# Kernel optimization log

Hardware: AMD Instinct MI355X
Metric: run time of the kernel (lower is better)

Reference implementation:

```python
import jax, jax.numpy as jnp
import numpy as np

HIDDEN = 1024
HEADS = 16
HEAD_DIM = HIDDEN // HEADS
B, S = 4, 2048


def setup_inputs() -> dict:
    key = jax.random.key(0)
    ks = jax.random.split(key, 12)
    d = {
        "query": jax.random.normal(ks[0], (B, S, HIDDEN), jnp.float32),
        "key": jax.random.normal(ks[1], (B, S, HIDDEN), jnp.float32),
        "value": jax.random.normal(ks[2], (B, S, HIDDEN), jnp.float32),
        "relative_time": jax.random.normal(ks[3], (B, 1, S, S), jnp.float32),
        # causal boolean mask (True = attend), matches masked_fill_(~mask)
        "attn_mask": jnp.broadcast_to(jnp.tril(jnp.ones((S, S), bool)), (B, S, S)),
    }
    scale = 1.0 / np.sqrt(HIDDEN)
    for i, name in enumerate(["q", "k", "v", "out"]):
        d[f"W{name}"] = jax.random.normal(ks[4 + 2 * i], (HIDDEN, HIDDEN), jnp.float32) * scale
        d[f"b{name}"] = jax.random.normal(ks[5 + 2 * i], (HIDDEN,), jnp.float32) * 0.01
    return d


def reference(query, key, value, relative_time, attn_mask,
              Wq, bq, Wk, bk, Wv, bv, Wout, bout):
    Bsz, Slen, _ = query.shape
    # linear projections (torch Linear: x @ W^T + b)
    Q = query @ Wq.T + bq
    K = key @ Wk.T + bk
    V = value @ Wv.T + bv
    # [B, H, S, Dh]
    Q = Q.reshape(Bsz, Slen, HEADS, HEAD_DIM).transpose(0, 2, 1, 3)
    K = K.reshape(Bsz, Slen, HEADS, HEAD_DIM).transpose(0, 2, 1, 3)
    V = V.reshape(Bsz, Slen, HEADS, HEAD_DIM).transpose(0, 2, 1, 3)

    scale = HEAD_DIM ** (-0.5)
    # scores: [B, H, S, S]; bias added BEFORE scaling, as in the original
    scores = jnp.einsum("bhqd,bhkd->bhqk", Q, K)
    scores = (scores + relative_time) * scale
    scores = jnp.where(attn_mask[:, None, :, :], scores, -jnp.inf)
    attn = jax.nn.softmax(scores, axis=-1)
    attn = jnp.nan_to_num(attn, nan=0.0)  # fully-masked rows -> 0
    # dropout: inference mode (training=False) -> identity
    out = jnp.einsum("bhqk,bhkd->bhqd", attn, V)
    out = out.transpose(0, 2, 1, 3).reshape(Bsz, Slen, HIDDEN)
    return out @ Wout.T + bout
```

## Files before the change

kernel.cpp:

```cpp
#include <hip/hip_runtime.h>


#define SEQ 2048
#define NH 16
#define DH 64
#define HID 1024
#define QSCALE 0.18033688011112f

typedef short bf16x8 __attribute__((ext_vector_type(8)));
typedef float f32x4  __attribute__((ext_vector_type(4)));
typedef unsigned short u16;
typedef unsigned short u16x4 __attribute__((ext_vector_type(4)));
typedef unsigned short u16x8 __attribute__((ext_vector_type(8)));

__device__ __forceinline__ float b2f(u16 u) {
    union { unsigned i; float f; } x; x.i = ((unsigned)u) << 16; return x.f;
}
__device__ __forceinline__ u16 f2b(float f) {
    union { float f; unsigned i; } x; x.f = f;
    unsigned r = x.i + 0x7fffu + ((x.i >> 16) & 1u);
    return (u16)(r >> 16);
}

typedef const __attribute__((address_space(1))) unsigned int guint;
typedef __attribute__((address_space(3))) unsigned int luint;
__device__ __forceinline__ void gload_lds16(const u16* g, u16* l) {
    __builtin_amdgcn_global_load_lds((guint*)g, (luint*)l, 16, 0, 0);
}

__global__ __launch_bounds__(256) void cvt_bf16_kernel(
    const float* __restrict__ in, u16* __restrict__ out, int n8)
{
    int i = blockIdx.x * 256 + threadIdx.x;
    const int stride = gridDim.x * 256;
    for (; i < n8; i += stride) {
        f32x4 a = *(const f32x4*)(in + (size_t)i * 8);
        f32x4 b = *(const f32x4*)(in + (size_t)i * 8 + 4);
        u16x8 o;
#pragma unroll
        for (int j = 0; j < 4; ++j) { o[j] = f2b(a[j]); o[j + 4] = f2b(b[j]); }
        *(u16x8*)(out + (size_t)i * 8) = o;
    }
}

__global__ __launch_bounds__(256) void rel_perm_kernel(
    const float* __restrict__ rel, u16* __restrict__ out)
{
    __shared__ u16 pl[4096];
    const int t   = threadIdx.x;
    const int blk = blockIdx.x;
    const int b   = blk >> 10;
    const int qc  = (blk >> 5) & 31;
    const int kc  = blk & 31;
    const int qloc  = t >> 2;
    const int kloc0 = (t & 3) << 4;

    const float* src = rel + ((size_t)b * SEQ + qc * 64 + qloc) * SEQ + kc * 64 + kloc0;
    const int qt   = qloc >> 4;
    const int quad = (qloc >> 2) & 3;
    const int g    = qloc & 3;
    const int nt   = t & 3;
    u16* dst = pl + qt * 1024 + quad * 256 + nt * 4 + g;
#pragma unroll
    for (int c = 0; c < 4; ++c) {
        f32x4 x = *(const f32x4*)(src + c * 4);
#pragma unroll
        for (int j = 0; j < 4; ++j)
            dst[(c * 4 + j) * 16] = f2b(x[j] * QSCALE);
    }
    __syncthreads();
    const size_t obase = (((size_t)b * 128 + qc * 4) * 32 + kc) * 1024;
#pragma unroll
    for (int q2 = 0; q2 < 4; ++q2)
        *(u16x4*)(out + obase + (size_t)q2 * 32768 + t * 4) =
            *(const u16x4*)(pl + q2 * 1024 + t * 4);
}

__global__ __launch_bounds__(256) void qkv_proj_kernel(
    const u16* __restrict__ xq, const u16* __restrict__ xk, const u16* __restrict__ xv,
    const u16* __restrict__ wq, const u16* __restrict__ wk, const u16* __restrict__ wv,
    const float* __restrict__ bq, const float* __restrict__ bk, const float* __restrict__ bv,
    u16* __restrict__ Qw, u16* __restrict__ Kw, u16* __restrict__ Vw)
{
    __shared__ __align__(16) u16 As[128 * 32];
    __shared__ __align__(16) u16 Bs[128 * 32];

    const int tid  = threadIdx.x;
    const int w    = tid >> 6;
    const int lane = tid & 63;
    const int l16  = lane & 15;
    const int quad = lane >> 4;

    const int bid = blockIdx.x;
    const int sel = bid >> 9;
    const int rem = bid & 511;
    const int tm = rem >> 3, tn = rem & 7;
    const int m0 = tm << 7, n0 = tn << 7;

    const u16* X    = sel == 0 ? xq : (sel == 1 ? xk : xv);
    const u16* W    = sel == 0 ? wq : (sel == 1 ? wk : wv);
    const float* bias = sel == 0 ? bq : (sel == 1 ? bk : bv);

    const int crow = lane >> 2;
    const int cofs = (lane & 3) << 3;

    f32x4 acc[4][4];
    const f32x4 zero = {0.f, 0.f, 0.f, 0.f};
#pragma unroll
    for (int r = 0; r < 4; ++r)
#pragma unroll
        for (int c = 0; c < 4; ++c) acc[r][c] = zero;

    const int wr = (w >> 1) << 6;
    const int wc = (w & 1) << 6;

    for (int k0 = 0; k0 < 1024; k0 += 32) {
#pragma unroll
        for (int c = 0; c < 2; ++c) {
            const int ch  = w + c * 4;
            const int row = ch * 16 + crow;
            gload_lds16(X + (size_t)(m0 + row) * 1024 + k0 + cofs, As + ch * 512 + lane * 8);
            gload_lds16(W + (size_t)(n0 + row) * 1024 + k0 + cofs, Bs + ch * 512 + lane * 8);
        }
        __syncthreads();
        bf16x8 a[4], b[4];
#pragma unroll
        for (int r = 0; r < 4; ++r) a[r] = *(const bf16x8*)(As + (wr + r * 16 + l16) * 32 + quad * 8);
#pragma unroll
        for (int c = 0; c < 4; ++c) b[c] = *(const bf16x8*)(Bs + (wc + c * 16 + l16) * 32 + quad * 8);
#pragma unroll
        for (int r = 0; r < 4; ++r)
#pragma unroll
            for (int c = 0; c < 4; ++c)
                acc[r][c] = __builtin_amdgcn_mfma_f32_16x16x32_bf16(a[r], b[c], acc[r][c], 0, 0, 0);
        __syncthreads();
    }

#pragma unroll
    for (int c = 0; c < 4; ++c) {
        const int n = n0 + wc + c * 16 + l16;
        const float bn = bias[n];
        const int h = n >> 6, d = n & 63;
#pragma unroll
        for (int r = 0; r < 4; ++r) {
#pragma unroll
            for (int g = 0; g < 4; ++g) {
                const int m  = m0 + wr + r * 16 + quad * 4 + g;
                const int b_ = m >> 11, s_ = m & 2047;
                const float val = acc[r][c][g] + bn;
                if (sel == 0)
                    Qw[(((size_t)(b_ * 16 + h)) * 2048 + s_) * 64 + d] = f2b(val * QSCALE);
                else if (sel == 1)
                    Kw[(((size_t)(b_ * 16 + h)) * 2048 + s_) * 64 + d] = f2b(val);
                else
                    Vw[(((size_t)(b_ * 16 + h)) * 64 + d) * 2048 + s_] = f2b(val);
            }
        }
    }
}

__global__ __launch_bounds__(512, 4) void attn_kernel(
    const u16* __restrict__ Qb, const u16* __restrict__ Kb,
    const u16* __restrict__ Vb, const u16* __restrict__ relb,
    u16* __restrict__ Ob)
{
    __shared__ __align__(16) u16 lds[18432];
    u16* Ks = lds;
    u16* Vt = lds + 4608;

    const int tid  = threadIdx.x;
    const int w    = tid >> 6;
    const int lane = tid & 63;
    const int l16  = lane & 15;
    const int quad = lane >> 4;
    u16* Pl = lds + 9216 + w * 1152;

    const int bh = blockIdx.x & 63;
    const int p  = blockIdx.x >> 6;
    const int b  = bh >> 4, h = bh & 15;

    const u16* Qp = Qb + (size_t)bh * SEQ * DH;
    const u16* Kg = Kb + (size_t)bh * SEQ * DH;
    const u16* Vg = Vb + (size_t)bh * DH * SEQ;

    const int r0 = tid >> 3, o0 = (tid & 7) << 3;

    for (int sidx = 0; sidx < 2; ++sidx) {
        const int qb  = sidx ? (15 - p) : p;
        const int q0w = qb * 128 + w * 16;

        bf16x8 qa[2];
#pragma unroll
        for (int ks = 0; ks < 2; ++ks)
            qa[ks] = *(const bf16x8*)(Qp + (size_t)(q0w + l16) * 64 + ks * 32 + quad * 8);

        f32x4 o[4], mrow, lrow;
        const f32x4 zero = {0.f, 0.f, 0.f, 0.f};
        const f32x4 ninf = {-1e30f, -1e30f, -1e30f, -1e30f};
        mrow = ninf; lrow = zero;
#pragma unroll
        for (int dt = 0; dt < 4; ++dt) o[dt] = zero;

        const int ntiles  = qb * 2 + 2;
        const int mytiles = qb * 2 + (w >> 2) + 1;

        const u16* relW = relb + ((size_t)(b * 128 + (q0w >> 4))) * 32768 + (size_t)lane * 16;

        bf16x8 kreg = *(const bf16x8*)(Kg + (size_t)r0 * 64 + o0);
        bf16x8 vreg = *(const bf16x8*)(Vg + (size_t)r0 * 2048 + o0);
        bf16x8 rr0 = *(const bf16x8*)(relW);
        bf16x8 rr1 = *(const bf16x8*)(relW + 8);

        for (int kt = 0; kt < ntiles; ++kt) {
            const int k0 = kt << 6;
            *(bf16x8*)(Ks + r0 * 72 + o0) = kreg;
            *(bf16x8*)(Vt + r0 * 72 + o0) = vreg;

            f32x4 s[4];
            if (kt < mytiles) {
#pragma unroll
                for (int nt = 0; nt < 4; ++nt)
#pragma unroll
                    for (int g = 0; g < 4; ++g)
                        s[nt][g] = b2f((u16)((nt < 2 ? rr0 : rr1)[(nt & 1) * 4 + g]));
            }

            const int ktn = (kt + 1 < ntiles) ? kt + 1 : kt;
            const int kn  = ktn << 6;
            kreg = *(const bf16x8*)(Kg + (size_t)(kn + r0) * 64 + o0);
            vreg = *(const bf16x8*)(Vg + (size_t)r0 * 2048 + kn + o0);
            rr0  = *(const bf16x8*)(relW + (size_t)ktn * 1024);
            rr1  = *(const bf16x8*)(relW + (size_t)ktn * 1024 + 8);
            __syncthreads();

            if (kt < mytiles) {
#pragma unroll
                for (int nt = 0; nt < 4; ++nt) {
                    bf16x8 kb0 = *(const bf16x8*)(Ks + (nt * 16 + l16) * 72 + quad * 8);
                    bf16x8 kb1 = *(const bf16x8*)(Ks + (nt * 16 + l16) * 72 + 32 + quad * 8);
                    s[nt] = __builtin_amdgcn_mfma_f32_16x16x32_bf16(qa[0], kb0, s[nt], 0, 0, 0);
                    s[nt] = __builtin_amdgcn_mfma_f32_16x16x32_bf16(qa[1], kb1, s[nt], 0, 0, 0);
                }
                if (kt == mytiles - 1) {
#pragma unroll
                    for (int nt = 0; nt < 4; ++nt)
#pragma unroll
                        for (int g = 0; g < 4; ++g) {
                            const int q = q0w + quad * 4 + g;
                            const int k = k0 + nt * 16 + l16;
                            if (k > q) s[nt][g] = -1e30f;
                        }
                }
                {
                    f32x4 t;
#pragma unroll
                    for (int g = 0; g < 4; ++g)
                        t[g] = fmaxf(fmaxf(s[0][g], s[1][g]), fmaxf(s[2][g], s[3][g]));
#pragma unroll
                    for (int off = 1; off < 16; off <<= 1)
#pragma unroll
                        for (int g = 0; g < 4; ++g)
                            t[g] = fmaxf(t[g], __shfl_xor(t[g], off, 64));
                    f32x4 mn, alpha;
#pragma unroll
                    for (int g = 0; g < 4; ++g) {
                        mn[g] = fmaxf(mrow[g], t[g]);
                        alpha[g] = __builtin_amdgcn_exp2f(mrow[g] - mn[g]);
                    }
                    mrow = mn;
#pragma unroll
                    for (int g = 0; g < 4; ++g) lrow[g] *= alpha[g];
#pragma unroll
                    for (int dt = 0; dt < 4; ++dt)
#pragma unroll
                        for (int g = 0; g < 4; ++g) o[dt][g] *= alpha[g];
#pragma unroll
                    for (int nt = 0; nt < 4; ++nt)
#pragma unroll
                        for (int g = 0; g < 4; ++g)
                            s[nt][g] = __builtin_amdgcn_exp2f(s[nt][g] - mn[g]);
                    f32x4 rs;
#pragma unroll
                    for (int g = 0; g < 4; ++g)
                        rs[g] = (s[0][g] + s[1][g]) + (s[2][g] + s[3][g]);
#pragma unroll
                    for (int off = 1; off < 16; off <<= 1)
#pragma unroll
                        for (int g = 0; g < 4; ++g)
                            rs[g] += __shfl_xor(rs[g], off, 64);
#pragma unroll
                    for (int g = 0; g < 4; ++g) lrow[g] += rs[g];
                }
#pragma unroll
                for (int nt = 0; nt < 4; ++nt)
#pragma unroll
                    for (int g = 0; g < 4; ++g)
                        Pl[(quad * 4 + g) * 72 + nt * 16 + l16] = f2b(s[nt][g]);
                bf16x8 pa[2];
#pragma unroll
                for (int ks = 0; ks < 2; ++ks)
                    pa[ks] = *(const bf16x8*)(Pl + l16 * 72 + ks * 32 + quad * 8);
#pragma unroll
                for (int dt = 0; dt < 4; ++dt) {
                    bf16x8 vb0 = *(const bf16x8*)(Vt + (dt * 16 + l16) * 72 + quad * 8);
                    bf16x8 vb1 = *(const bf16x8*)(Vt + (dt * 16 + l16) * 72 + 32 + quad * 8);
                    o[dt] = __builtin_amdgcn_mfma_f32_16x16x32_bf16(pa[0], vb0, o[dt], 0, 0, 0);
                    o[dt] = __builtin_amdgcn_mfma_f32_16x16x32_bf16(pa[1], vb1, o[dt], 0, 0, 0);
                }
            }
            __syncthreads();
        }

        {
            f32x4 linv;
#pragma unroll
            for (int g = 0; g < 4; ++g) linv[g] = 1.0f / lrow[g];
#pragma unroll
            for (int dt = 0; dt < 4; ++dt)
#pragma unroll
                for (int g = 0; g < 4; ++g)
                    Pl[(quad * 4 + g) * 72 + dt * 16 + l16] = f2b(o[dt][g] * linv[g]);
        }
#pragma unroll
        for (int pp = 0; pp < 2; ++pp) {
            const int c = lane + pp * 64;
            const int row = c >> 3, col = (c & 7) << 3;
            bf16x8 t = *(const bf16x8*)(Pl + row * 72 + col);
            *(bf16x8*)(Ob + ((size_t)b * SEQ + q0w + row) * HID + h * DH + col) = t;
        }
    }
}

__global__ __launch_bounds__(256) void out_proj_kernel(
    const u16* __restrict__ X, const u16* __restrict__ W,
    const float* __restrict__ bias, float* __restrict__ out)
{
    __shared__ __align__(16) u16 As[128 * 32];
    __shared__ __align__(16) u16 Bs[128 * 32];

    const int tid  = threadIdx.x;
    const int w    = tid >> 6;
    const int lane = tid & 63;
    const int l16  = lane & 15;
    const int quad = lane >> 4;

    const int bid = blockIdx.x;
    const int tm = bid >> 3, tn = bid & 7;
    const int m0 = tm << 7, n0 = tn << 7;

    const int crow = lane >> 2;
    const int cofs = (lane & 3) << 3;

    f32x4 acc[4][4];
    const f32x4 zero = {0.f, 0.f, 0.f, 0.f};
#pragma unroll
    for (int r = 0; r < 4; ++r)
#pragma unroll
        for (int c = 0; c < 4; ++c) acc[r][c] = zero;

    const int wr = (w >> 1) << 6;
    const int wc = (w & 1) << 6;

    for (int k0 = 0; k0 < 1024; k0 += 32) {
#pragma unroll
        for (int c = 0; c < 2; ++c) {
            const int ch  = w + c * 4;
            const int row = ch * 16 + crow;
            gload_lds16(X + (size_t)(m0 + row) * 1024 + k0 + cofs, As + ch * 512 + lane * 8);
            gload_lds16(W + (size_t)(n0 + row) * 1024 + k0 + cofs, Bs + ch * 512 + lane * 8);
        }
        __syncthreads();
        bf16x8 a[4], b[4];
#pragma unroll
        for (int r = 0; r < 4; ++r) a[r] = *(const bf16x8*)(As + (wr + r * 16 + l16) * 32 + quad * 8);
#pragma unroll
        for (int c = 0; c < 4; ++c) b[c] = *(const bf16x8*)(Bs + (wc + c * 16 + l16) * 32 + quad * 8);
#pragma unroll
        for (int r = 0; r < 4; ++r)
#pragma unroll
            for (int c = 0; c < 4; ++c)
                acc[r][c] = __builtin_amdgcn_mfma_f32_16x16x32_bf16(a[r], b[c], acc[r][c], 0, 0, 0);
        __syncthreads();
    }

#pragma unroll
    for (int c = 0; c < 4; ++c) {
        const int n = n0 + wc + c * 16 + l16;
        const float bn = bias[n];
#pragma unroll
        for (int r = 0; r < 4; ++r) {
#pragma unroll
            for (int g = 0; g < 4; ++g) {
                const int m = m0 + wr + r * 16 + quad * 4 + g;
                out[(size_t)m * 1024 + n] = acc[r][c][g] + bn;
            }
        }
    }
}

extern "C" void kernel_launch(void* const* d_in, const int* in_sizes, int n_in,
                              void* d_out, int out_size, void* d_ws, size_t ws_size,
                              hipStream_t stream)
{
    const float* q   = (const float*)d_in[0];
    const float* k   = (const float*)d_in[1];
    const float* v   = (const float*)d_in[2];
    const float* rel = (const float*)d_in[3];
    const float* wq = (const float*)d_in[5];  const float* bq = (const float*)d_in[6];
    const float* wk = (const float*)d_in[7];  const float* bk = (const float*)d_in[8];
    const float* wv = (const float*)d_in[9];  const float* bv = (const float*)d_in[10];
    const float* wo = (const float*)d_in[11]; const float* bo = (const float*)d_in[12];

    u16* ws = (u16*)d_ws;
    u16* Qw   = ws;
    u16* Kw   = ws + 8388608ULL;
    u16* Vw   = ws + 16777216ULL;
    u16* Ow   = ws + 25165824ULL;
    u16* relb = ws + 33554432ULL;

    u16* Xqb = Ow;
    u16* Xkb = relb;
    u16* Xvb = relb + 8388608ULL;
    u16* Wqb = (u16*)d_out;
    u16* Wkb = Wqb + 1048576ULL;
    u16* Wvb = Wqb + 2097152ULL;
    u16* Wob = Qw;

    cvt_bf16_kernel<<<1024, 256, 0, stream>>>(q, Xqb, 1048576);
    cvt_bf16_kernel<<<1024, 256, 0, stream>>>(k, Xkb, 1048576);
    cvt_bf16_kernel<<<1024, 256, 0, stream>>>(v, Xvb, 1048576);
    cvt_bf16_kernel<<<512, 256, 0, stream>>>(wq, Wqb, 131072);
    cvt_bf16_kernel<<<512, 256, 0, stream>>>(wk, Wkb, 131072);
    cvt_bf16_kernel<<<512, 256, 0, stream>>>(wv, Wvb, 131072);

    qkv_proj_kernel<<<1536, 256, 0, stream>>>(Xqb, Xkb, Xvb, Wqb, Wkb, Wvb,
                                              bq, bk, bv, Qw, Kw, Vw);
    rel_perm_kernel<<<4096, 256, 0, stream>>>(rel, relb);
    attn_kernel<<<512, 512, 0, stream>>>(Qw, Kw, Vw, relb, Ow);
    cvt_bf16_kernel<<<512, 256, 0, stream>>>(wo, Wob, 131072);
    out_proj_kernel<<<512, 256, 0, stream>>>(Ow, Wob, bo, (float*)d_out);
}
```

Baseline: 484.5 us.

## Double-buffer swizzled K/V LDS tiles and defer softmax row-sum reduction

K and V tiles now go into two alternating LDS buffers, so each key-tile iteration needs one barrier instead of two. The padded row stride of 72 is replaced by an XOR swizzle on 64-wide rows to avoid bank conflicts. The per-tile cross-lane shuffle reduction of the softmax denominator is dropped: each lane keeps a rescaled partial sum, and the lanes are reduced once after the loop. LDS use per block grows to about 50 KB, which may cap how many blocks fit on a CU below the four in the launch bounds.

```diff
diff --git a/kernel.cpp b/kernel.cpp
--- a/kernel.cpp
+++ b/kernel.cpp
@@ -159,21 +159,20 @@
     }
 }
 
+#define SWZ(R, C) (((R) << 6) + ((((C) ^ ((R) & 7))) << 3))
+
 __global__ __launch_bounds__(512, 4) void attn_kernel(
     const u16* __restrict__ Qb, const u16* __restrict__ Kb,
     const u16* __restrict__ Vb, const u16* __restrict__ relb,
     u16* __restrict__ Ob)
 {
-    __shared__ __align__(16) u16 lds[18432];
-    u16* Ks = lds;
-    u16* Vt = lds + 4608;
-
+    __shared__ __align__(16) u16 lds[25600];
     const int tid  = threadIdx.x;
     const int w    = tid >> 6;
     const int lane = tid & 63;
     const int l16  = lane & 15;
     const int quad = lane >> 4;
-    u16* Pl = lds + 9216 + w * 1152;
+    u16* Pl = lds + 16384 + w * 1152;
 
     const int bh = blockIdx.x & 63;
     const int p  = blockIdx.x >> 6;
@@ -183,7 +182,10 @@
     const u16* Kg = Kb + (size_t)bh * SEQ * DH;
     const u16* Vg = Vb + (size_t)bh * DH * SEQ;
 
-    const int r0 = tid >> 3, o0 = (tid & 7) << 3;
+    const int r0 = tid >> 3;
+    const int c0 = tid & 7;
+    const int o0 = c0 << 3;
+    const int sw0 = ((c0 ^ (r0 & 7)) << 3);
 
     for (int sidx = 0; sidx < 2; ++sidx) {
         const int qb  = sidx ? (15 - p) : p;
@@ -213,11 +215,14 @@
 
         for (int kt = 0; kt < ntiles; ++kt) {
             const int k0 = kt << 6;
-            *(bf16x8*)(Ks + r0 * 72 + o0) = kreg;
-            *(bf16x8*)(Vt + r0 * 72 + o0) = vreg;
-
+            u16* Ksb = lds + ((kt & 1) << 12);
+            u16* Vtb = lds + 8192 + ((kt & 1) << 12);
+            *(bf16x8*)(Ksb + r0 * 64 + sw0) = kreg;
+            *(bf16x8*)(Vtb + r0 * 64 + sw0) = vreg;
+
+            const bool act = kt < mytiles;
             f32x4 s[4];
-            if (kt < mytiles) {
+            if (act) {
 #pragma unroll
                 for (int nt = 0; nt < 4; ++nt)
 #pragma unroll
@@ -231,13 +236,15 @@
             vreg = *(const bf16x8*)(Vg + (size_t)r0 * 2048 + kn + o0);
             rr0  = *(const bf16x8*)(relW + (size_t)ktn * 1024);
             rr1  = *(const bf16x8*)(relW + (size_t)ktn * 1024 + 8);
+
             __syncthreads();
 
-            if (kt < mytiles) {
+            if (act) {
 #pragma unroll
                 for (int nt = 0; nt < 4; ++nt) {
-                    bf16x8 kb0 = *(const bf16x8*)(Ks + (nt * 16 + l16) * 72 + quad * 8);
-                    bf16x8 kb1 = *(const bf16x8*)(Ks + (nt * 16 + l16) * 72 + 32 + quad * 8);
+                    const int R = nt * 16 + l16;
+                    bf16x8 kb0 = *(const bf16x8*)(Ksb + SWZ(R, quad));
+                    bf16x8 kb1 = *(const bf16x8*)(Ksb + SWZ(R, 4 | quad));
                     s[nt] = __builtin_amdgcn_mfma_f32_16x16x32_bf16(qa[0], kb0, s[nt], 0, 0, 0);
                     s[nt] = __builtin_amdgcn_mfma_f32_16x16x32_bf16(qa[1], kb1, s[nt], 0, 0, 0);
                 }
@@ -269,8 +276,6 @@
                     }
                     mrow = mn;
 #pragma unroll
-                    for (int g = 0; g < 4; ++g) lrow[g] *= alpha[g];
-#pragma unroll
                     for (int dt = 0; dt < 4; ++dt)
 #pragma unroll
                         for (int g = 0; g < 4; ++g) o[dt][g] *= alpha[g];
@@ -279,17 +284,10 @@
 #pragma unroll
                         for (int g = 0; g < 4; ++g)
                             s[nt][g] = __builtin_amdgcn_exp2f(s[nt][g] - mn[g]);
-                    f32x4 rs;
 #pragma unroll
                     for (int g = 0; g < 4; ++g)
-                        rs[g] = (s[0][g] + s[1][g]) + (s[2][g] + s[3][g]);
-#pragma unroll
-                    for (int off = 1; off < 16; off <<= 1)
-#pragma unroll
-                        for (int g = 0; g < 4; ++g)
-                            rs[g] += __shfl_xor(rs[g], off, 64);
-#pragma unroll
-                    for (int g = 0; g < 4; ++g) lrow[g] += rs[g];
+                        lrow[g] = lrow[g] * alpha[g]
+                                + ((s[0][g] + s[1][g]) + (s[2][g] + s[3][g]));
                 }
 #pragma unroll
                 for (int nt = 0; nt < 4; ++nt)
@@ -302,15 +300,20 @@
                     pa[ks] = *(const bf16x8*)(Pl + l16 * 72 + ks * 32 + quad * 8);
 #pragma unroll
                 for (int dt = 0; dt < 4; ++dt) {
-                    bf16x8 vb0 = *(const bf16x8*)(Vt + (dt * 16 + l16) * 72 + quad * 8);
-                    bf16x8 vb1 = *(const bf16x8*)(Vt + (dt * 16 + l16) * 72 + 32 + quad * 8);
+                    const int R = dt * 16 + l16;
+                    bf16x8 vb0 = *(const bf16x8*)(Vtb + SWZ(R, quad));
+                    bf16x8 vb1 = *(const bf16x8*)(Vtb + SWZ(R, 4 | quad));
                     o[dt] = __builtin_amdgcn_mfma_f32_16x16x32_bf16(pa[0], vb0, o[dt], 0, 0, 0);
                     o[dt] = __builtin_amdgcn_mfma_f32_16x16x32_bf16(pa[1], vb1, o[dt], 0, 0, 0);
                 }
             }
-            __syncthreads();
-        }
-
+        }
+
+#pragma unroll
+        for (int off = 1; off < 16; off <<= 1)
+#pragma unroll
+            for (int g = 0; g < 4; ++g)
+                lrow[g] += __shfl_xor(lrow[g], off, 64);
         {
             f32x4 linv;
 #pragma unroll
```

Result: faster. 460.5 us (-5.0%).
